# Performance work log

Hardware: AMD Instinct MI355X
Metric: run time of the kernel (lower is better)

The kernel has to match this reference:

```python
import jax, jax.numpy as jnp
import numpy as np

DIM = 2048
HEADS = 32
WINDOW = 8   # local_attn
B = 4
N = 197


def _local_mask(w, n):
    # Faithful to local_attention(): for row i, columns j in [max(i-w,0), min(i+w, n))
    # get weight (w - |i-j|/2)/w; everything else is 0 (later masked to -inf).
    i = jnp.arange(n)[:, None]
    j = jnp.arange(n)[None, :]
    d = jnp.abs(i - j).astype(jnp.float32)
    in_win = (j >= i - w) & (j < i + w)  # range(start, end) excludes i+w
    return jnp.where(in_win, (w - d / 2.0) / w, 0.0)  # (N, N)


def setup_inputs() -> dict:
    key = jax.random.key(0)
    k1, k2, k3, k4 = jax.random.split(key, 4)
    x = jax.random.normal(k1, (B, N, DIM), dtype=jnp.float32)
    qkv_w = jax.random.normal(k2, (3 * DIM, DIM), dtype=jnp.float32) * 0.02  # no qkv bias
    proj_w = jax.random.normal(k3, (DIM, DIM), dtype=jnp.float32) * 0.02
    proj_b = jax.random.normal(k4, (DIM,), dtype=jnp.float32) * 0.02
    return {"x": x, "qkv_w": qkv_w, "proj_w": proj_w, "proj_b": proj_b}


def reference(x, qkv_w, proj_w, proj_b):
    Bb, Nn, C = x.shape
    H = HEADS
    hd = C // H
    scale = hd ** (-0.5)
    # qkv projection: (B, N, 3C) -> (3, B, H, N, hd)
    qkv = (x @ qkv_w.T).reshape(Bb, Nn, 3, H, hd).transpose(2, 0, 3, 1, 4)
    q, k, v = qkv[0], qkv[1], qkv[2]
    attn = jnp.einsum('bhnd,bhmd->bhnm', q, k) * scale  # (B, H, N, N)
    m = _local_mask(WINDOW, Nn)  # (N, N), broadcasts over B, H
    # attn * mask, then masked_fill(mask == 0, -inf), then softmax
    attn = jnp.where(m != 0.0, attn * m, -jnp.inf)
    attn = jax.nn.softmax(attn, axis=-1)
    out = jnp.einsum('bhnm,bhmd->bhnd', attn, v)  # (B, H, N, hd)
    out = out.transpose(0, 2, 1, 3).reshape(Bb, Nn, C)
    return out @ proj_w.T + proj_b
```

## Files before the change

### kernel.cpp

```cpp
#include <hip/hip_runtime.h>
#include <math.h>

#define B_SZ   4
#define N_SEQ  197
#define DIMC   2048
#define HEADS  32
#define HD     64
#define WIN    8
#define M_ROWS (B_SZ * N_SEQ)
#define M_PAD  896

using f32x4 = __attribute__((ext_vector_type(4))) float;
using s16x8 = __attribute__((ext_vector_type(8))) short;

__device__ inline ushort f2bf(float f) {
  uint x = __float_as_uint(f);
  uint r = (x + 0x7fffu + ((x >> 16) & 1u)) >> 16;
  return (ushort)r;
}
__device__ inline float bf2f(ushort u) {
  return __uint_as_float(((uint)u) << 16);
}

__device__ inline void gload16(const ushort* g, ushort* l) {
  __builtin_amdgcn_global_load_lds(
      (const __attribute__((address_space(1))) unsigned int*)g,
      (__attribute__((address_space(3))) unsigned int*)l, 16, 0, 0);
}

#define NX (M_ROWS * DIMC / 8)
#define NQ (3 * DIMC * DIMC / 8)
#define NP (DIMC * DIMC / 8)

__global__ __launch_bounds__(256)
void cvt_all(const float* __restrict__ x,  const float* __restrict__ qw,
             const float* __restrict__ pw, ushort* __restrict__ xb,
             ushort* __restrict__ qwb, ushort* __restrict__ pwb) {
  int i = blockIdx.x * 256 + threadIdx.x;
  const float* src; ushort* dst; int idx;
  if (i < NX)                { src = x;  dst = xb;  idx = i; }
  else if (i < NX + NQ)      { src = qw; dst = qwb; idx = i - NX; }
  else if (i < NX + NQ + NP) { src = pw; dst = pwb; idx = i - NX - NQ; }
  else return;
  f32x4 a = ((const f32x4*)src)[2 * idx];
  f32x4 b = ((const f32x4*)src)[2 * idx + 1];
  ushort4 u0, u1;
  u0.x = f2bf(a.x); u0.y = f2bf(a.y); u0.z = f2bf(a.z); u0.w = f2bf(a.w);
  u1.x = f2bf(b.x); u1.y = f2bf(b.y); u1.z = f2bf(b.z); u1.w = f2bf(b.w);
  ((ushort4*)dst)[2 * idx]     = u0;
  ((ushort4*)dst)[2 * idx + 1] = u1;
}

__global__ __launch_bounds__(256, 3)
void gemm_bt_bf16(const ushort* __restrict__ A, const ushort* __restrict__ Bw,
                  ushort* __restrict__ Cout,
                  int Mdim, int Ndim, int Kfull, int Ksplit) {
  __shared__ ushort As[3][128 * 32];
  __shared__ ushort Bs[3][128 * 32];
  const int tid  = threadIdx.x;
  const int lane = tid & 63;
  const int wave = tid >> 6;

  const int nwg  = gridDim.x * gridDim.y;
  const int phys = blockIdx.y * gridDim.x + blockIdx.x;
  const int cpx  = nwg >> 3;
  const int lg   = (phys & 7) * cpx + (phys >> 3);
  const int m0 = (lg % gridDim.x) * 128;
  const int n0 = (lg / gridDim.x) * 128;
  const int koff = blockIdx.z * Ksplit;
  ushort* C = Cout + (size_t)blockIdx.z * Mdim * Ndim;

  const int wr = (wave >> 1) * 64;
  const int wc = (wave & 1) * 64;
  const int fr = lane & 15;
  const int kg = lane >> 4;
  const int srow = lane >> 2;
  const int scol = ((lane & 3) ^ ((srow >> 1) & 3)) * 8;
  const int rdA  = (kg ^ ((fr >> 1) & 3)) * 8;

  f32x4 acc[4][4];
#pragma unroll
  for (int i = 0; i < 4; ++i)
#pragma unroll
    for (int j = 0; j < 4; ++j)
      acc[i][j] = (f32x4){0.f, 0.f, 0.f, 0.f};

  const ushort* Asrc0 = A  + (size_t)(m0 + wave * 32 + srow)      * Kfull + koff + scol;
  const ushort* Asrc1 = A  + (size_t)(m0 + wave * 32 + 16 + srow) * Kfull + koff + scol;
  const ushort* Bsrc0 = Bw + (size_t)(n0 + wave * 32 + srow)      * Kfull + koff + scol;
  const ushort* Bsrc1 = Bw + (size_t)(n0 + wave * 32 + 16 + srow) * Kfull + koff + scol;

  const int nt = Ksplit >> 5;

  auto STAGE = [&](int kk, int b) {
    const int k = kk << 5;
    gload16(Asrc0 + k, &As[b][wave * 1024]);
    gload16(Asrc1 + k, &As[b][wave * 1024 + 512]);
    gload16(Bsrc0 + k, &Bs[b][wave * 1024]);
    gload16(Bsrc1 + k, &Bs[b][wave * 1024 + 512]);
  };

  STAGE(0, 0);
  STAGE(1, 1);

  int cur = 0, s2 = 2;
  for (int t = 0; t < nt; ++t) {
    if (t < nt - 1) asm volatile("s_waitcnt vmcnt(4)" ::: "memory");
    else            asm volatile("s_waitcnt vmcnt(0)" ::: "memory");
    __builtin_amdgcn_s_barrier();
    __builtin_amdgcn_sched_barrier(0);

    if (t + 2 < nt) STAGE(t + 2, s2);

    s16x8 af[4], bfr[4];
#pragma unroll
    for (int i = 0; i < 4; ++i)
      af[i] = *(const s16x8*)(&As[cur][(wr + i * 16 + fr) * 32 + rdA]);
#pragma unroll
    for (int j = 0; j < 4; ++j)
      bfr[j] = *(const s16x8*)(&Bs[cur][(wc + j * 16 + fr) * 32 + rdA]);
    __builtin_amdgcn_s_setprio(1);
#pragma unroll
    for (int i = 0; i < 4; ++i)
#pragma unroll
      for (int j = 0; j < 4; ++j)
        acc[i][j] = __builtin_amdgcn_mfma_f32_16x16x32_bf16(af[i], bfr[j], acc[i][j], 0, 0, 0);
    __builtin_amdgcn_s_setprio(0);

    cur += 1; if (cur >= 3) cur -= 3;
    s2  += 1; if (s2  >= 3) s2  -= 3;
  }

  const int crow_base = m0 + wr + kg * 4;
  const int ccol_base = n0 + wc + fr;
#pragma unroll
  for (int j = 0; j < 4; ++j) {
    int col = ccol_base + j * 16;
#pragma unroll
    for (int i = 0; i < 4; ++i)
#pragma unroll
      for (int r = 0; r < 4; ++r) {
        int grow = crow_base + i * 16 + r;
        if (grow < Mdim) C[(size_t)grow * Ndim + col] = f2bf(acc[i][j][r]);
      }
  }
}

__global__ __launch_bounds__(256)
void local_attn(const ushort* __restrict__ p0, const ushort* __restrict__ p1,
                ushort* __restrict__ ao) {
  const int gw = blockIdx.x * 4 + (threadIdx.x >> 6);
  if (gw >= B_SZ * HEADS * N_SEQ) return;
  const int lane = threadIdx.x & 63;
  const int h = gw % HEADS;
  const int t = gw / HEADS;
  const int i = t % N_SEQ;
  const int b = t / N_SEQ;
  const int row = b * N_SEQ + i;
  const size_t stride = 3 * DIMC;

  const size_t qi = (size_t)row * stride + h * HD + lane;
  const float q = (bf2f(p0[qi]) + bf2f(p1[qi])) * 0.125f;
  int j0 = i - WIN; if (j0 < 0) j0 = 0;
  int j1 = i + WIN; if (j1 > N_SEQ) j1 = N_SEQ;

  float s[16];
#pragma unroll
  for (int jj = 0; jj < 16; ++jj) {
    int j = j0 + jj;
    bool ok = (j < j1);
    int jc = ok ? j : (j1 - 1);
    size_t ki = (size_t)(b * N_SEQ + jc) * stride + DIMC + h * HD + lane;
    float kd = bf2f(p0[ki]) + bf2f(p1[ki]);
    float p = q * kd;
#pragma unroll
    for (int o = 32; o > 0; o >>= 1) p += __shfl_xor(p, o);
    float d = fabsf((float)(i - j));
    float m = 1.0f - d * 0.0625f;
    s[jj] = ok ? p * m : -INFINITY;
  }

  float mx = -INFINITY;
#pragma unroll
  for (int jj = 0; jj < 16; ++jj) mx = fmaxf(mx, s[jj]);
  float sum = 0.f;
#pragma unroll
  for (int jj = 0; jj < 16; ++jj) { float e = expf(s[jj] - mx); s[jj] = e; sum += e; }
  const float inv = 1.f / sum;

  float o = 0.f;
#pragma unroll
  for (int jj = 0; jj < 16; ++jj) {
    int j = j0 + jj;
    if (j < j1) {
      size_t vi = (size_t)(b * N_SEQ + j) * stride + 2 * DIMC + h * HD + lane;
      o += s[jj] * (bf2f(p0[vi]) + bf2f(p1[vi]));
    }
  }
  ao[(size_t)row * DIMC + h * HD + lane] = f2bf(o * inv);
}

#define NR8 (M_ROWS * DIMC / 8)
__global__ __launch_bounds__(256)
void reduce4_bias(const ushort* __restrict__ parts, const float* __restrict__ bias,
                  float* __restrict__ out) {
  int i = blockIdx.x * 256 + threadIdx.x;
  if (i >= NR8) return;
  const size_t slice = (size_t)M_ROWS * DIMC;
  float a[8];
#pragma unroll
  for (int e = 0; e < 8; ++e) a[e] = 0.f;
#pragma unroll
  for (int z = 0; z < 4; ++z) {
    s16x8 v = *(const s16x8*)(parts + z * slice + (size_t)i * 8);
#pragma unroll
    for (int e = 0; e < 8; ++e) a[e] += bf2f((ushort)v[e]);
  }
  const int col = (i * 8) & (DIMC - 1);
  f32x4 b0 = *(const f32x4*)(bias + col);
  f32x4 b1 = *(const f32x4*)(bias + col + 4);
  f32x4 o0 = {a[0] + b0.x, a[1] + b0.y, a[2] + b0.z, a[3] + b0.w};
  f32x4 o1 = {a[4] + b1.x, a[5] + b1.y, a[6] + b1.z, a[7] + b1.w};
  ((f32x4*)out)[2 * i]     = o0;
  ((f32x4*)out)[2 * i + 1] = o1;
}

extern "C" void kernel_launch(void* const* d_in, const int* in_sizes, int n_in,
                              void* d_out, int out_size, void* d_ws, size_t ws_size,
                              hipStream_t stream) {
  const float* x      = (const float*)d_in[0];
  const float* qkv_w  = (const float*)d_in[1];
  const float* proj_w = (const float*)d_in[2];
  const float* proj_b = (const float*)d_in[3];
  float* out = (float*)d_out;

  char* p = (char*)d_ws;
  ushort* x_bf    = (ushort*)p;  p += (size_t)M_PAD * DIMC * 2;
  ushort* qkvw_bf = (ushort*)p;  p += (size_t)3 * DIMC * DIMC * 2;
  ushort* projw_bf= (ushort*)p;  p += (size_t)DIMC * DIMC * 2;
  ushort* qkv_p   = (ushort*)p;  p += (size_t)2 * M_ROWS * 3 * DIMC * 2;
  ushort* ao_bf   = (ushort*)p;  p += (size_t)M_PAD * DIMC * 2;
  ushort* proj_p  = (ushort*)p;

  dim3 blk(256);

  {
    int total = NX + NQ + NP;
    cvt_all<<<dim3((total + 255) / 256), blk, 0, stream>>>(
        x, qkv_w, proj_w, x_bf, qkvw_bf, projw_bf);
  }

  gemm_bt_bf16<<<dim3(M_PAD / 128, (3 * DIMC) / 128, 2), blk, 0, stream>>>(
      x_bf, qkvw_bf, qkv_p, M_ROWS, 3 * DIMC, DIMC, DIMC / 2);

  int total_waves = B_SZ * HEADS * N_SEQ;
  local_attn<<<dim3((total_waves + 3) / 4), blk, 0, stream>>>(
      qkv_p, qkv_p + (size_t)M_ROWS * 3 * DIMC, ao_bf);

  gemm_bt_bf16<<<dim3(M_PAD / 128, DIMC / 128, 4), blk, 0, stream>>>(
      ao_bf, projw_bf, proj_p, M_ROWS, DIMC, DIMC, DIMC / 4);

  reduce4_bias<<<dim3((NR8 + 255) / 256), blk, 0, stream>>>(proj_p, proj_b, out);
}
```

Measured before the change: 106.6 us.

## Parallelize local attention across keys with vectorized loads and LDS reduction

Restructures the local attention kernel so each wavefront lane handles one key position and a 16-element slice of the head dimension, instead of every lane looping over all 16 keys. Q, K and V are read with 16-byte vector loads, the dot products are reduced with a few shuffles, and softmax max and sum use cross-lane shuffles with the fast exp intrinsic. The weighted V contributions go through per-wave shared memory and are summed per output lane. This cuts serial shuffle-reduction chains and scalar loads, but adds LDS traffic and relies on the wave being synchronized without a barrier.

```diff
diff --git a/kernel.cpp b/kernel.cpp
--- a/kernel.cpp
+++ b/kernel.cpp
@@ -149,9 +149,13 @@
 __global__ __launch_bounds__(256)
 void local_attn(const ushort* __restrict__ p0, const ushort* __restrict__ p1,
                 ushort* __restrict__ ao) {
-  const int gw = blockIdx.x * 4 + (threadIdx.x >> 6);
+  __shared__ float plds[4][16][68];
+  const int wv = threadIdx.x >> 6;
+  const int gw = blockIdx.x * 4 + wv;
   if (gw >= B_SZ * HEADS * N_SEQ) return;
   const int lane = threadIdx.x & 63;
+  const int jj = lane >> 2;
+  const int ds = lane & 3;
   const int h = gw % HEADS;
   const int t = gw / HEADS;
   const int i = t % N_SEQ;
@@ -159,44 +163,89 @@
   const int row = b * N_SEQ + i;
   const size_t stride = 3 * DIMC;
 
-  const size_t qi = (size_t)row * stride + h * HD + lane;
-  const float q = (bf2f(p0[qi]) + bf2f(p1[qi])) * 0.125f;
   int j0 = i - WIN; if (j0 < 0) j0 = 0;
   int j1 = i + WIN; if (j1 > N_SEQ) j1 = N_SEQ;
-
-  float s[16];
-#pragma unroll
-  for (int jj = 0; jj < 16; ++jj) {
-    int j = j0 + jj;
-    bool ok = (j < j1);
-    int jc = ok ? j : (j1 - 1);
-    size_t ki = (size_t)(b * N_SEQ + jc) * stride + DIMC + h * HD + lane;
-    float kd = bf2f(p0[ki]) + bf2f(p1[ki]);
-    float p = q * kd;
-#pragma unroll
-    for (int o = 32; o > 0; o >>= 1) p += __shfl_xor(p, o);
+  const int j = j0 + jj;
+  const bool ok = (j < j1);
+  const int jc = ok ? j : (j1 - 1);
+
+  float qs[16];
+  {
+    const size_t qi = (size_t)row * stride + h * HD + ds * 16;
+    s16x8 a0 = *(const s16x8*)(p0 + qi);
+    s16x8 a1 = *(const s16x8*)(p0 + qi + 8);
+    s16x8 b0 = *(const s16x8*)(p1 + qi);
+    s16x8 b1 = *(const s16x8*)(p1 + qi + 8);
+#pragma unroll
+    for (int e = 0; e < 8; ++e) {
+      qs[e]     = (bf2f((ushort)a0[e]) + bf2f((ushort)b0[e])) * 0.125f;
+      qs[8 + e] = (bf2f((ushort)a1[e]) + bf2f((ushort)b1[e])) * 0.125f;
+    }
+  }
+
+  float s;
+  {
+    const size_t ki = (size_t)(b * N_SEQ + jc) * stride + DIMC + h * HD + ds * 16;
+    s16x8 a0 = *(const s16x8*)(p0 + ki);
+    s16x8 a1 = *(const s16x8*)(p0 + ki + 8);
+    s16x8 b0 = *(const s16x8*)(p1 + ki);
+    s16x8 b1 = *(const s16x8*)(p1 + ki + 8);
+    float acc = 0.f;
+#pragma unroll
+    for (int e = 0; e < 8; ++e) {
+      acc += qs[e]     * (bf2f((ushort)a0[e]) + bf2f((ushort)b0[e]));
+      acc += qs[8 + e] * (bf2f((ushort)a1[e]) + bf2f((ushort)b1[e]));
+    }
+    s = acc;
+  }
+  s += __shfl_xor(s, 1);
+  s += __shfl_xor(s, 2);
+
+  {
     float d = fabsf((float)(i - j));
     float m = 1.0f - d * 0.0625f;
-    s[jj] = ok ? p * m : -INFINITY;
-  }
-
-  float mx = -INFINITY;
-#pragma unroll
-  for (int jj = 0; jj < 16; ++jj) mx = fmaxf(mx, s[jj]);
-  float sum = 0.f;
-#pragma unroll
-  for (int jj = 0; jj < 16; ++jj) { float e = expf(s[jj] - mx); s[jj] = e; sum += e; }
+    s = ok ? s * m : -INFINITY;
+  }
+
+  float mx = s;
+  mx = fmaxf(mx, __shfl_xor(mx, 4));
+  mx = fmaxf(mx, __shfl_xor(mx, 8));
+  mx = fmaxf(mx, __shfl_xor(mx, 16));
+  mx = fmaxf(mx, __shfl_xor(mx, 32));
+  float e = __expf(s - mx);
+  float sum = e;
+  sum += __shfl_xor(sum, 4);
+  sum += __shfl_xor(sum, 8);
+  sum += __shfl_xor(sum, 16);
+  sum += __shfl_xor(sum, 32);
   const float inv = 1.f / sum;
 
+  {
+    const size_t vi = (size_t)(b * N_SEQ + jc) * stride + 2 * DIMC + h * HD + ds * 16;
+    s16x8 a0 = *(const s16x8*)(p0 + vi);
+    s16x8 a1 = *(const s16x8*)(p0 + vi + 8);
+    s16x8 b0 = *(const s16x8*)(p1 + vi);
+    s16x8 b1 = *(const s16x8*)(p1 + vi + 8);
+    const float ee = ok ? e : 0.f;
+    f32x4 w0, w1, w2, w3;
+#pragma unroll
+    for (int g = 0; g < 4; ++g) {
+      w0[g] = ee * (bf2f((ushort)a0[g])     + bf2f((ushort)b0[g]));
+      w1[g] = ee * (bf2f((ushort)a0[4 + g]) + bf2f((ushort)b0[4 + g]));
+      w2[g] = ee * (bf2f((ushort)a1[g])     + bf2f((ushort)b1[g]));
+      w3[g] = ee * (bf2f((ushort)a1[4 + g]) + bf2f((ushort)b1[4 + g]));
+    }
+    *(f32x4*)&plds[wv][jj][ds * 16]      = w0;
+    *(f32x4*)&plds[wv][jj][ds * 16 + 4]  = w1;
+    *(f32x4*)&plds[wv][jj][ds * 16 + 8]  = w2;
+    *(f32x4*)&plds[wv][jj][ds * 16 + 12] = w3;
+  }
+  asm volatile("s_waitcnt lgkmcnt(0)" ::: "memory");
+  __builtin_amdgcn_sched_barrier(0);
+
   float o = 0.f;
 #pragma unroll
-  for (int jj = 0; jj < 16; ++jj) {
-    int j = j0 + jj;
-    if (j < j1) {
-      size_t vi = (size_t)(b * N_SEQ + j) * stride + 2 * DIMC + h * HD + lane;
-      o += s[jj] * (bf2f(p0[vi]) + bf2f(p1[vi]));
-    }
-  }
+  for (int q = 0; q < 16; ++q) o += plds[wv][q][lane];
   ao[(size_t)row * DIMC + h * HD + lane] = f2bf(o * inv);
 }
 
```

Result: faster. 86.90 us (-18.4%).
